# Optimization experiments

Hardware: AMD Instinct MI355X
Metric: run time of the kernel (lower is better)

Reference implementation:

```python
import jax, jax.numpy as jnp
import numpy as np

_JPEG_QUANT_TABLE = np.array([
    [16, 11, 10, 16, 24, 40, 51, 61],
    [12, 12, 14, 19, 26, 58, 60, 55],
    [14, 13, 16, 24, 40, 57, 69, 56],
    [14, 17, 22, 29, 51, 87, 80, 62],
    [18, 22, 37, 56, 68, 109, 103, 77],
    [24, 35, 55, 64, 81, 104, 113, 92],
    [49, 64, 78, 87, 103, 121, 120, 101],
    [72, 92, 95, 98, 112, 100, 103, 99]], dtype=np.float32)


def _dct_matrix():
    # Orthonormal 8x8 DCT-II basis: D[k, i] = alpha(k) * cos(pi*(2i+1)k/16)
    n = 8
    k = np.arange(n)[:, None].astype(np.float64)
    i = np.arange(n)[None, :].astype(np.float64)
    alpha = np.where(k == 0, np.sqrt(1.0 / n), np.sqrt(2.0 / n))
    return jnp.asarray(alpha * np.cos(np.pi * (2 * i + 1) * k / (2 * n)), dtype=jnp.float32)


def setup_inputs() -> dict:
    key = jax.random.key(0)
    image = jax.random.uniform(key, (32, 3, 512, 512), dtype=jnp.float32)
    return {"image": image, "quality": 75}


def reference(image, quality):
    B, C, H, W = image.shape  # H, W divisible by 8 (no padding branch needed)
    bh, bw = H // 8, W // 8

    # libjpeg quality -> scale (quality is a static Python int)
    scale = 5000.0 / quality if quality < 50 else 200.0 - 2.0 * quality
    qtable = jnp.clip(jnp.asarray(_JPEG_QUANT_TABLE) * scale / 100.0, 1.0, 255.0)
    dct = _dct_matrix()

    x = image - 0.5
    # blockify: (B,C,H,W) -> (B*C, bh, bw, 8, 8)
    blocks = x.reshape(B * C, bh, 8, bw, 8).transpose(0, 1, 3, 2, 4)

    # 2D DCT: dct @ block @ dct^T
    dct_blocks = jnp.einsum('ki,...ij,lj->...kl', dct, blocks, dct)

    # quantize with straight-through estimator (forward: round, backward: identity)
    normalized = dct_blocks / qtable
    quantized = normalized + jax.lax.stop_gradient(jnp.round(normalized) - normalized)
    dequantized = quantized * qtable

    # 2D IDCT: dct^T @ block @ dct
    spatial = jnp.einsum('ki,...kl,lj->...ij', dct, dequantized, dct)

    # deblockify: (B*C, bh, bw, 8, 8) -> (B, C, H, W)
    result = spatial.transpose(0, 1, 3, 2, 4).reshape(B, C, H, W)
    return jnp.clip(result + 0.5, 0.0, 1.0)
```

## Files before the change

### kernel.cpp

```cpp
#include <hip/hip_runtime.h>


static __device__ __constant__ float c_qbase[64] = {
    16.f, 11.f, 10.f, 16.f, 24.f, 40.f, 51.f, 61.f,
    12.f, 12.f, 14.f, 19.f, 26.f, 58.f, 60.f, 55.f,
    14.f, 13.f, 16.f, 24.f, 40.f, 57.f, 69.f, 56.f,
    14.f, 17.f, 22.f, 29.f, 51.f, 87.f, 80.f, 62.f,
    18.f, 22.f, 37.f, 56.f, 68.f, 109.f, 103.f, 77.f,
    24.f, 35.f, 55.f, 64.f, 81.f, 104.f, 113.f, 92.f,
    49.f, 64.f, 78.f, 87.f, 103.f, 121.f, 120.f, 101.f,
    72.f, 92.f, 95.f, 98.f, 112.f, 100.f, 103.f, 99.f
};

__global__ __launch_bounds__(256, 2)
void jpeg_fused_kernel(const float* __restrict__ in, const int* __restrict__ qual,
                       float* __restrict__ out, int nblk, int W) {
    constexpr float D[8][8] = {
        { 0.3535533906f,  0.3535533906f,  0.3535533906f,  0.3535533906f,
          0.3535533906f,  0.3535533906f,  0.3535533906f,  0.3535533906f },
        { 0.4903926402f,  0.4157348062f,  0.2777851165f,  0.0975451610f,
         -0.0975451610f, -0.2777851165f, -0.4157348062f, -0.4903926402f },
        { 0.4619397663f,  0.1913417162f, -0.1913417162f, -0.4619397663f,
         -0.4619397663f, -0.1913417162f,  0.1913417162f,  0.4619397663f },
        { 0.4157348062f, -0.0975451610f, -0.4903926402f, -0.2777851165f,
          0.2777851165f,  0.4903926402f,  0.0975451610f, -0.4157348062f },
        { 0.3535533906f, -0.3535533906f, -0.3535533906f,  0.3535533906f,
          0.3535533906f, -0.3535533906f, -0.3535533906f,  0.3535533906f },
        { 0.2777851165f, -0.4903926402f,  0.0975451610f,  0.4157348062f,
         -0.4157348062f, -0.0975451610f,  0.4903926402f, -0.2777851165f },
        { 0.1913417162f, -0.4619397663f,  0.4619397663f, -0.1913417162f,
         -0.1913417162f,  0.4619397663f, -0.4619397663f,  0.1913417162f },
        { 0.0975451610f, -0.2777851165f,  0.4157348062f, -0.4903926402f,
          0.4903926402f, -0.4157348062f,  0.2777851165f, -0.0975451610f }
    };

    __shared__ float qlds[64];
    if (threadIdx.x < 64) {
        int q = qual[0];
        double sd = (q < 50) ? (5000.0 / (double)q) : (200.0 - 2.0 * (double)q);
        float scale = (float)sd;
        float v = c_qbase[threadIdx.x] * scale / 100.0f;
        qlds[threadIdx.x] = fminf(fmaxf(v, 1.0f), 255.0f);
    }
    __syncthreads();

    int t = blockIdx.x * 256 + threadIdx.x;
    if (t >= nblk) return;

    const int img = t >> 12;
    const int by  = (t >> 6) & 63;
    const int bx  = t & 63;
    const long base = ((long)img * 512 + (long)by * 8) * (long)W + (long)bx * 8;

    float X[8][8];
#pragma unroll
    for (int r = 0; r < 8; ++r) {
        const float4 a = *reinterpret_cast<const float4*>(in + base + (long)r * W);
        const float4 b = *reinterpret_cast<const float4*>(in + base + (long)r * W + 4);
        X[r][0] = a.x - 0.5f; X[r][1] = a.y - 0.5f; X[r][2] = a.z - 0.5f; X[r][3] = a.w - 0.5f;
        X[r][4] = b.x - 0.5f; X[r][5] = b.y - 0.5f; X[r][6] = b.z - 0.5f; X[r][7] = b.w - 0.5f;
    }

    float T[8][8];
#pragma unroll
    for (int k = 0; k < 8; ++k) {
#pragma unroll
        for (int j = 0; j < 8; ++j) {
            float s = 0.0f;
#pragma unroll
            for (int i = 0; i < 8; ++i) s = fmaf(D[k][i], X[i][j], s);
            T[k][j] = s;
        }
    }

#pragma unroll
    for (int k = 0; k < 8; ++k) {
        float y[8];
#pragma unroll
        for (int l = 0; l < 8; ++l) {
            float s = 0.0f;
#pragma unroll
            for (int j = 0; j < 8; ++j) s = fmaf(T[k][j], D[l][j], s);
            const float qv = qlds[k * 8 + l];
            y[l] = rintf(s / qv) * qv;
        }
#pragma unroll
        for (int j = 0; j < 8; ++j) {
            float s = 0.0f;
#pragma unroll
            for (int l = 0; l < 8; ++l) s = fmaf(y[l], D[l][j], s);
            T[k][j] = s;
        }
    }

#pragma unroll
    for (int i = 0; i < 8; ++i) {
        float srow[8];
#pragma unroll
        for (int j = 0; j < 8; ++j) {
            float s = 0.0f;
#pragma unroll
            for (int k = 0; k < 8; ++k) s = fmaf(D[k][i], T[k][j], s);
            s += 0.5f;
            srow[j] = fminf(fmaxf(s, 0.0f), 1.0f);
        }
        float4 a = make_float4(srow[0], srow[1], srow[2], srow[3]);
        float4 b = make_float4(srow[4], srow[5], srow[6], srow[7]);
        *reinterpret_cast<float4*>(out + base + (long)i * W)     = a;
        *reinterpret_cast<float4*>(out + base + (long)i * W + 4) = b;
    }
}

extern "C" void kernel_launch(void* const* d_in, const int* in_sizes, int n_in,
                              void* d_out, int out_size, void* d_ws, size_t ws_size,
                              hipStream_t stream) {
    const float* img  = (const float*)d_in[0];
    const int*   qual = (const int*)d_in[1];
    float*       out  = (float*)d_out;

    const int W = 512;
    const int nblk = out_size / 64;
    const int nthreads = 256;
    const int ngrid = (nblk + nthreads - 1) / nthreads;

    jpeg_fused_kernel<<<ngrid, nthreads, 0, stream>>>(img, qual, out, nblk, W);
}
```

Baseline: 41.55 us.

## Split each 8x8 DCT block across eight row threads with LDS transposes

New measurement: 36.01 us. 13.3% less time.

```diff
diff --git a/kernel.cpp b/kernel.cpp
--- a/kernel.cpp
+++ b/kernel.cpp
@@ -12,9 +12,11 @@
     72.f, 92.f, 95.f, 98.f, 112.f, 100.f, 103.f, 99.f
 };
 
-__global__ __launch_bounds__(256, 2)
-void jpeg_fused_kernel(const float* __restrict__ in, const int* __restrict__ qual,
-                       float* __restrict__ out, int nblk, int W) {
+#define LDS_PITCH 9
+
+__global__ __launch_bounds__(256, 8)
+void jpeg_row_kernel(const float* __restrict__ in, const int* __restrict__ qual,
+                     float* __restrict__ out) {
     constexpr float D[8][8] = {
         { 0.3535533906f,  0.3535533906f,  0.3535533906f,  0.3535533906f,
           0.3535533906f,  0.3535533906f,  0.3535533906f,  0.3535533906f },
@@ -35,6 +37,8 @@
     };
 
     __shared__ float qlds[64];
+    __shared__ float tr[256 * LDS_PITCH];
+
     if (threadIdx.x < 64) {
         int q = qual[0];
         double sd = (q < 50) ? (5000.0 / (double)q) : (200.0 - 2.0 * (double)q);
@@ -44,71 +48,79 @@
     }
     __syncthreads();
 
-    int t = blockIdx.x * 256 + threadIdx.x;
-    if (t >= nblk) return;
+    const int tid = threadIdx.x;
+    const int gt  = blockIdx.x * 256 + tid;
+    const int b   = gt >> 3;
+    const int r   = gt & 7;
+    const int img = b >> 12;
+    const int by  = (b >> 6) & 63;
+    const int bx  = b & 63;
+    const long rowaddr = (((long)img * 512 + (long)by * 8 + r) * 512) + (long)bx * 8;
 
-    const int img = t >> 12;
-    const int by  = (t >> 6) & 63;
-    const int bx  = t & 63;
-    const long base = ((long)img * 512 + (long)by * 8) * (long)W + (long)bx * 8;
+    float qc[8];
+#pragma unroll
+    for (int k = 0; k < 8; ++k) qc[k] = qlds[k * 8 + r];
 
-    float X[8][8];
-#pragma unroll
-    for (int r = 0; r < 8; ++r) {
-        const float4 a = *reinterpret_cast<const float4*>(in + base + (long)r * W);
-        const float4 b = *reinterpret_cast<const float4*>(in + base + (long)r * W + 4);
-        X[r][0] = a.x - 0.5f; X[r][1] = a.y - 0.5f; X[r][2] = a.z - 0.5f; X[r][3] = a.w - 0.5f;
-        X[r][4] = b.x - 0.5f; X[r][5] = b.y - 0.5f; X[r][6] = b.z - 0.5f; X[r][7] = b.w - 0.5f;
+    float x[8];
+    {
+        const float4 a  = *reinterpret_cast<const float4*>(in + rowaddr);
+        const float4 b4 = *reinterpret_cast<const float4*>(in + rowaddr + 4);
+        x[0] = a.x - 0.5f; x[1] = a.y - 0.5f; x[2] = a.z - 0.5f; x[3] = a.w - 0.5f;
+        x[4] = b4.x - 0.5f; x[5] = b4.y - 0.5f; x[6] = b4.z - 0.5f; x[7] = b4.w - 0.5f;
     }
 
-    float T[8][8];
+    float u[8];
+#pragma unroll
+    for (int l = 0; l < 8; ++l) {
+        float s = 0.0f;
+#pragma unroll
+        for (int j = 0; j < 8; ++j) s = fmaf(x[j], D[l][j], s);
+        u[l] = s;
+    }
+
+    const int base_w = tid * LDS_PITCH;
+    const int base_r = (tid & ~7) * LDS_PITCH;
+#pragma unroll
+    for (int j = 0; j < 8; ++j) tr[base_w + j] = u[j];
+    float t[8];
+#pragma unroll
+    for (int j = 0; j < 8; ++j) t[j] = tr[base_r + j * LDS_PITCH + r];
+
+    float y[8];
 #pragma unroll
     for (int k = 0; k < 8; ++k) {
+        float s = 0.0f;
 #pragma unroll
-        for (int j = 0; j < 8; ++j) {
-            float s = 0.0f;
+        for (int j = 0; j < 8; ++j) s = fmaf(D[k][j], t[j], s);
+        y[k] = rintf(s / qc[k]) * qc[k];
+    }
+
+    float v[8];
 #pragma unroll
-            for (int i = 0; i < 8; ++i) s = fmaf(D[k][i], X[i][j], s);
-            T[k][j] = s;
-        }
+    for (int j = 0; j < 8; ++j) {
+        float s = 0.0f;
+#pragma unroll
+        for (int k = 0; k < 8; ++k) s = fmaf(D[k][j], y[k], s);
+        v[j] = s;
     }
 
 #pragma unroll
-    for (int k = 0; k < 8; ++k) {
-        float y[8];
+    for (int j = 0; j < 8; ++j) tr[base_w + j] = v[j];
+    float w[8];
 #pragma unroll
-        for (int l = 0; l < 8; ++l) {
-            float s = 0.0f;
+    for (int j = 0; j < 8; ++j) w[j] = tr[base_r + j * LDS_PITCH + r];
+
+    float srow[8];
 #pragma unroll
-            for (int j = 0; j < 8; ++j) s = fmaf(T[k][j], D[l][j], s);
-            const float qv = qlds[k * 8 + l];
-            y[l] = rintf(s / qv) * qv;
-        }
+    for (int c = 0; c < 8; ++c) {
+        float s = 0.0f;
 #pragma unroll
-        for (int j = 0; j < 8; ++j) {
-            float s = 0.0f;
-#pragma unroll
-            for (int l = 0; l < 8; ++l) s = fmaf(y[l], D[l][j], s);
-            T[k][j] = s;
-        }
+        for (int l = 0; l < 8; ++l) s = fmaf(w[l], D[l][c], s);
+        s += 0.5f;
+        srow[c] = fminf(fmaxf(s, 0.0f), 1.0f);
     }
-
-#pragma unroll
-    for (int i = 0; i < 8; ++i) {
-        float srow[8];
-#pragma unroll
-        for (int j = 0; j < 8; ++j) {
-            float s = 0.0f;
-#pragma unroll
-            for (int k = 0; k < 8; ++k) s = fmaf(D[k][i], T[k][j], s);
-            s += 0.5f;
-            srow[j] = fminf(fmaxf(s, 0.0f), 1.0f);
-        }
-        float4 a = make_float4(srow[0], srow[1], srow[2], srow[3]);
-        float4 b = make_float4(srow[4], srow[5], srow[6], srow[7]);
-        *reinterpret_cast<float4*>(out + base + (long)i * W)     = a;
-        *reinterpret_cast<float4*>(out + base + (long)i * W + 4) = b;
-    }
+    *reinterpret_cast<float4*>(out + rowaddr)     = make_float4(srow[0], srow[1], srow[2], srow[3]);
+    *reinterpret_cast<float4*>(out + rowaddr + 4) = make_float4(srow[4], srow[5], srow[6], srow[7]);
 }
 
 extern "C" void kernel_launch(void* const* d_in, const int* in_sizes, int n_in,
@@ -118,10 +130,9 @@
     const int*   qual = (const int*)d_in[1];
     float*       out  = (float*)d_out;
 
-    const int W = 512;
-    const int nblk = out_size / 64;
-    const int nthreads = 256;
-    const int ngrid = (nblk + nthreads - 1) / nthreads;
+    const int nthreads_total = (out_size / 64) * 8;
+    const int block = 256;
+    const int grid = nthreads_total / block;
 
-    jpeg_fused_kernel<<<ngrid, nthreads, 0, stream>>>(img, qual, out, nblk, W);
+    jpeg_row_kernel<<<grid, block, 0, stream>>>(img, qual, out);
 }
```
